# Performance work log

Measured on AMD Instinct MI355X. Metric: run time of the kernel, lower is better.

## Reference

```python
import jax, jax.numpy as jnp
import numpy as np

N_NODES = 50000
N_EDGES = 1600000
IN_CH = 128
HEADS = 4
OUT_PER_HEAD = 32  # out_channels // heads with concat=True
NEG_SLOPE = 0.2    # GATConv default leaky_relu slope
SOFTMAX_EPS = 1e-16  # PyG scatter-softmax denominator eps
LN_EPS = 1e-5


def setup_inputs() -> dict:
    key = jax.random.key(0)
    ks = jax.random.split(key, 8)
    x = jax.random.normal(ks[0], (N_NODES, IN_CH), dtype=jnp.float32)
    edge_index = jax.random.randint(ks[1], (2, N_EDGES), 0, N_NODES, dtype=jnp.int32)
    W = jax.random.normal(ks[2], (IN_CH, HEADS * OUT_PER_HEAD), dtype=jnp.float32) * (1.0 / np.sqrt(IN_CH))
    att_src = jax.random.normal(ks[3], (HEADS, OUT_PER_HEAD), dtype=jnp.float32) * 0.1
    att_dst = jax.random.normal(ks[4], (HEADS, OUT_PER_HEAD), dtype=jnp.float32) * 0.1
    bias = jnp.zeros((HEADS * OUT_PER_HEAD,), dtype=jnp.float32)
    gamma = jnp.ones((HEADS * OUT_PER_HEAD,), dtype=jnp.float32)
    beta = jnp.zeros((HEADS * OUT_PER_HEAD,), dtype=jnp.float32)
    return {"x": x, "edge_index": edge_index, "W": W, "att_src": att_src,
            "att_dst": att_dst, "bias": bias, "gamma": gamma, "beta": beta}


def reference(x, edge_index, W, att_src, att_dst, bias, gamma, beta):
    N = x.shape[0]
    H, C = att_src.shape
    # GATConv default add_self_loops=True
    loop = jnp.arange(N, dtype=edge_index.dtype)
    src = jnp.concatenate([edge_index[0], loop])  # message source j
    dst = jnp.concatenate([edge_index[1], loop])  # aggregation target i

    h = (x @ W).reshape(N, H, C)                      # [N,H,C]
    a_s = jnp.einsum('nhc,hc->nh', h, att_src)        # [N,H]
    a_d = jnp.einsum('nhc,hc->nh', h, att_dst)        # [N,H]

    logits = jax.nn.leaky_relu(a_s[src] + a_d[dst], NEG_SLOPE)  # [E,H]
    # segment softmax over edges grouped by destination node
    m = jax.ops.segment_max(logits, dst, num_segments=N)        # [N,H]
    m = jnp.where(jnp.isfinite(m), m, 0.0)
    e = jnp.exp(logits - m[dst])
    s = jax.ops.segment_sum(e, dst, num_segments=N)             # [N,H]
    alpha = e / (s[dst] + SOFTMAX_EPS)                          # [E,H]

    msg = h[src] * alpha[:, :, None]                            # [E,H,C]
    out = jax.ops.segment_sum(msg, dst, num_segments=N)         # [N,H,C]
    out = out.reshape(N, H * C) + bias

    mu = out.mean(axis=-1, keepdims=True)
    var = ((out - mu) ** 2).mean(axis=-1, keepdims=True)
    y = (out - mu) / jnp.sqrt(var + LN_EPS) * gamma + beta
    return jax.nn.elu(y)
```

## Files before the change

### kernel.cpp

```cpp
#include <hip/hip_runtime.h>
#include <hip/hip_bf16.h>

typedef __hip_bfloat16 bf16;
typedef unsigned int u32;
typedef unsigned short u16;

constexpr int N   = 50000;
constexpr int E   = 1600000;
constexpr int C   = 128;
constexpr int H   = 4;
constexpr int NB  = 782;
constexpr int CAP = 2560;
constexpr int CHUNK = 4096;
constexpr float NEG  = 0.2f;
constexpr float SEPS = 1e-16f;
constexpr float LEPS = 1e-5f;

__device__ __forceinline__ float lo16(u32 v) { return __uint_as_float(v << 16); }
__device__ __forceinline__ float hi16(u32 v) { return __uint_as_float(v & 0xFFFF0000u); }

__global__ __launch_bounds__(256) void k1_gemm(
    const float* __restrict__ x, const float* __restrict__ W,
    const float* __restrict__ att_s, const float* __restrict__ att_d,
    bf16* __restrict__ hb, float* __restrict__ as_, float* __restrict__ ad_)
{
    const int nb = blockIdx.x * 16;
    const int t  = threadIdx.x;
    __shared__ float sx[16 * 128];
    const float4* xg = (const float4*)(x + nb * 128);
    ((float4*)sx)[t]       = xg[t];
    ((float4*)sx)[t + 256] = xg[t + 256];
    __syncthreads();

    const int c = t & 127;
    const int g = t >> 7;
    const float* xb = sx + (g << 10);
    float acc[8] = {0.f, 0.f, 0.f, 0.f, 0.f, 0.f, 0.f, 0.f};

    for (int k = 0; k < 128; k += 4) {
        const float w0 = W[(k + 0) * 128 + c];
        const float w1 = W[(k + 1) * 128 + c];
        const float w2 = W[(k + 2) * 128 + c];
        const float w3 = W[(k + 3) * 128 + c];
#pragma unroll
        for (int j = 0; j < 8; ++j) {
            const float4 xv = *(const float4*)(xb + j * 128 + k);
            acc[j] = fmaf(xv.x, w0, fmaf(xv.y, w1, fmaf(xv.z, w2, fmaf(xv.w, w3, acc[j]))));
        }
    }

    const int lane = t & 63;
    const int head = c >> 5;
    const float asc = att_s[c], adc = att_d[c];
#pragma unroll
    for (int j = 0; j < 8; ++j) {
        const int node = nb + (g << 3) + j;
        hb[node * 128 + c] = __float2bfloat16(acc[j]);
        float vs = acc[j] * asc;
        float vd = acc[j] * adc;
#pragma unroll
        for (int off = 16; off; off >>= 1) {
            vs += __shfl_xor(vs, off, 64);
            vd += __shfl_xor(vd, off, 64);
        }
        if ((lane & 31) == 0) {
            as_[node * H + head] = vs;
            ad_[node * H + head] = vd;
        }
    }
}

__global__ __launch_bounds__(256) void kbin(
    const int* __restrict__ ei, u32* __restrict__ gcur, u32* __restrict__ pairs)
{
    __shared__ u32 lcnt[NB], lbase[NB], lfill[NB];
    const int t = threadIdx.x;
    const int base = blockIdx.x * CHUNK;
    const int nE = min(CHUNK, E - base);
    for (int i = t; i < NB; i += 256) lcnt[i] = 0;
    __syncthreads();
    for (int i = t; i < nE; i += 256)
        atomicAdd(&lcnt[((u32)ei[E + base + i]) >> 6], 1u);
    __syncthreads();
    for (int i = t; i < NB; i += 256) {
        u32 cb = lcnt[i];
        lbase[i] = cb ? atomicAdd(&gcur[i], cb) : 0u;
        lfill[i] = 0u;
    }
    __syncthreads();
    for (int i = t; i < nE; i += 256) {
        u32 src = (u32)ei[base + i];
        u32 dst = (u32)ei[E + base + i];
        u32 b = dst >> 6;
        u32 pos = atomicAdd(&lfill[b], 1u);
        pairs[(size_t)b * CAP + lbase[b] + pos] = src | ((dst & 63u) << 16);
    }
}

__global__ __launch_bounds__(64) void kscan(
    const u32* __restrict__ gcur, u32* __restrict__ bbase, int* __restrict__ row_ptr)
{
    const int t = threadIdx.x;
    u32 vals[13];
    u32 s = 0;
#pragma unroll
    for (int i = 0; i < 13; ++i) {
        int idx = t * 13 + i;
        u32 v = (idx < NB) ? gcur[idx] : 0u;
        vals[i] = s; s += v;
    }
    u32 incl = s;
#pragma unroll
    for (int off = 1; off < 64; off <<= 1) {
        u32 u = __shfl_up(incl, off, 64);
        if (t >= off) incl += u;
    }
    const u32 excl = incl - s;
#pragma unroll
    for (int i = 0; i < 13; ++i) {
        int idx = t * 13 + i;
        if (idx < NB) bbase[idx] = excl + vals[i];
    }
    if (t == 0) row_ptr[N] = E;
}

__global__ __launch_bounds__(256) void kfill2(
    const u32* __restrict__ pairs, const u32* __restrict__ gcur,
    const u32* __restrict__ bbase, int* __restrict__ row_ptr, u16* __restrict__ col)
{
    __shared__ int jcnt[64], joff[64], jcur[64];
    const int b = blockIdx.x, t = threadIdx.x;
    const int cntb = (int)gcur[b];
    const int base = (int)bbase[b];
    if (t < 64) jcnt[t] = 0;
    __syncthreads();
    const u32* pr = pairs + (size_t)b * CAP;
    for (int i = t; i < cntb; i += 256) atomicAdd(&jcnt[pr[i] >> 16], 1);
    __syncthreads();
    if (t < 64) {
        int v = jcnt[t], incl = v;
#pragma unroll
        for (int off = 1; off < 64; off <<= 1) {
            int u = __shfl_up(incl, off, 64);
            if (t >= off) incl += u;
        }
        joff[t] = incl - v;
        const int n = b * 64 + t;
        if (n < N) row_ptr[n] = base + joff[t];
        jcur[t] = 0;
    }
    __syncthreads();
    for (int i = t; i < cntb; i += 256) {
        const u32 p = pr[i];
        const int j = p >> 16;
        const int pos = atomicAdd(&jcur[j], 1);
        col[base + joff[j] + pos] = (u16)(p & 0xFFFFu);
    }
}

__global__ __launch_bounds__(256) void kd_agg_ln(
    const int* __restrict__ row_ptr, const u16* __restrict__ col,
    const u32* __restrict__ hb, const float* __restrict__ as_,
    const float* __restrict__ ad_,
    const float* __restrict__ bias, const float* __restrict__ gamma,
    const float* __restrict__ beta, float* __restrict__ out)
{
    int gid = blockIdx.x * blockDim.x + threadIdx.x;
    int n = gid >> 6;
    if (n >= N) return;
    const int lane = gid & 63;
    const int head = lane >> 4;

    const float adn = ad_[n * H + head];
    float l = as_[n * H + head] + adn;
    l = fmaxf(l, NEG * l);
    float w = __expf(l);
    float den = w;
    u32 hv = hb[n * 64 + lane];
    float num0 = w * lo16(hv);
    float num1 = w * hi16(hv);

    int k = row_ptr[n];
    const int end = row_ptr[n + 1];
    for (; k + 4 <= end; k += 4) {
        const int s0 = col[k], s1 = col[k + 1], s2 = col[k + 2], s3 = col[k + 3];
        float l0 = as_[s0 * H + head] + adn;
        float l1 = as_[s1 * H + head] + adn;
        float l2 = as_[s2 * H + head] + adn;
        float l3 = as_[s3 * H + head] + adn;
        const u32 v0 = hb[s0 * 64 + lane];
        const u32 v1 = hb[s1 * 64 + lane];
        const u32 v2 = hb[s2 * 64 + lane];
        const u32 v3 = hb[s3 * 64 + lane];
        l0 = fmaxf(l0, NEG * l0); l1 = fmaxf(l1, NEG * l1);
        l2 = fmaxf(l2, NEG * l2); l3 = fmaxf(l3, NEG * l3);
        const float w0 = __expf(l0), w1 = __expf(l1);
        const float w2 = __expf(l2), w3 = __expf(l3);
        den += (w0 + w1) + (w2 + w3);
        num0 = fmaf(w0, lo16(v0), num0); num1 = fmaf(w0, hi16(v0), num1);
        num0 = fmaf(w1, lo16(v1), num0); num1 = fmaf(w1, hi16(v1), num1);
        num0 = fmaf(w2, lo16(v2), num0); num1 = fmaf(w2, hi16(v2), num1);
        num0 = fmaf(w3, lo16(v3), num0); num1 = fmaf(w3, hi16(v3), num1);
    }
    for (; k < end; ++k) {
        const int s = col[k];
        float ls = as_[s * H + head] + adn;
        ls = fmaxf(ls, NEG * ls);
        const float ws = __expf(ls);
        const u32 vs = hb[s * 64 + lane];
        den += ws;
        num0 = fmaf(ws, lo16(vs), num0);
        num1 = fmaf(ws, hi16(vs), num1);
    }

    const int c0 = lane * 2;
    const float inv_den = 1.f / (den + SEPS);
    float v0 = num0 * inv_den + bias[c0];
    float v1 = num1 * inv_den + bias[c0 + 1];

    float sum = v0 + v1;
#pragma unroll
    for (int off = 32; off; off >>= 1) sum += __shfl_xor(sum, off, 64);
    const float mu = sum * (1.0f / C);
    const float d0 = v0 - mu, d1 = v1 - mu;
    float sq = d0 * d0 + d1 * d1;
#pragma unroll
    for (int off = 32; off; off >>= 1) sq += __shfl_xor(sq, off, 64);
    const float inv = rsqrtf(sq * (1.0f / C) + LEPS);
    float y0 = d0 * inv * gamma[c0]     + beta[c0];
    float y1 = d1 * inv * gamma[c0 + 1] + beta[c0 + 1];
    y0 = y0 > 0.f ? y0 : __expf(y0) - 1.f;
    y1 = y1 > 0.f ? y1 : __expf(y1) - 1.f;
    float2 o; o.x = y0; o.y = y1;
    *(float2*)(out + (size_t)n * C + c0) = o;
}

extern "C" void kernel_launch(void* const* d_in, const int* in_sizes, int n_in,
                              void* d_out, int out_size, void* d_ws, size_t ws_size,
                              hipStream_t stream)
{
    const float* x     = (const float*)d_in[0];
    const int*   ei    = (const int*)  d_in[1];
    const float* W     = (const float*)d_in[2];
    const float* att_s = (const float*)d_in[3];
    const float* att_d = (const float*)d_in[4];
    const float* bias  = (const float*)d_in[5];
    const float* gamma = (const float*)d_in[6];
    const float* beta  = (const float*)d_in[7];
    float* out = (float*)d_out;

    char* p = (char*)d_ws;
    bf16*  hb      = (bf16*)p;   p += (size_t)N * C * sizeof(bf16);
    float* as_     = (float*)p;  p += (size_t)N * H * sizeof(float);
    float* ad_     = (float*)p;  p += (size_t)N * H * sizeof(float);
    u32*   pairs   = (u32*)p;    p += (size_t)NB * CAP * sizeof(u32);
    u16*   col     = (u16*)p;    p += ((size_t)E * sizeof(u16) + 15) & ~(size_t)15;
    int*   row_ptr = (int*)p;    p += ((size_t)(N + 1) * sizeof(int) + 15) & ~(size_t)15;
    u32*   gcur    = (u32*)p;    p += (size_t)NB * sizeof(u32);
    u32*   bbase   = (u32*)p;

    hipMemsetAsync(gcur, 0, NB * sizeof(u32), stream);
    k1_gemm<<<N / 16, 256, 0, stream>>>(x, W, att_s, att_d, hb, as_, ad_);
    kbin<<<(E + CHUNK - 1) / CHUNK, 256, 0, stream>>>(ei, gcur, pairs);
    kscan<<<1, 64, 0, stream>>>(gcur, bbase, row_ptr);
    kfill2<<<NB, 256, 0, stream>>>(pairs, gcur, bbase, row_ptr, col);
    kd_agg_ln<<<(N * 64) / 256, 256, 0, stream>>>(
        row_ptr, col, (const u32*)hb, as_, ad_, bias, gamma, beta, out);
}
```

Baseline: 245.4 us.

## Precompute per-edge attention weights in CSR fill and fold scan into fill kernel

The CSR fill kernel now computes the leaky-relu/exp attention weight for all four heads of each edge and stores them as fp16 next to the column index, so the aggregation kernel only gathers a weight instead of recomputing it per lane. The separate scan kernel is removed; each fill block sums the preceding bucket counts itself. The binning kernel caches destinations in shared memory instead of reading them twice, and the aggregation loop is unrolled to 8 edges. This trades an extra E*8-byte write and read plus fp16 rounding of the weights for less exp work and fewer scattered as_ gathers in the hot kernel.

```diff
diff --git a/kernel.cpp b/kernel.cpp
--- a/kernel.cpp
+++ b/kernel.cpp
@@ -1,9 +1,11 @@
 #include <hip/hip_runtime.h>
 #include <hip/hip_bf16.h>
+#include <hip/hip_fp16.h>
 
 typedef __hip_bfloat16 bf16;
 typedef unsigned int u32;
 typedef unsigned short u16;
+typedef unsigned long long u64;
 
 constexpr int N   = 50000;
 constexpr int E   = 1600000;
@@ -74,13 +76,17 @@
     const int* __restrict__ ei, u32* __restrict__ gcur, u32* __restrict__ pairs)
 {
     __shared__ u32 lcnt[NB], lbase[NB], lfill[NB];
+    __shared__ u16 dstl[CHUNK];
     const int t = threadIdx.x;
     const int base = blockIdx.x * CHUNK;
     const int nE = min(CHUNK, E - base);
     for (int i = t; i < NB; i += 256) lcnt[i] = 0;
     __syncthreads();
-    for (int i = t; i < nE; i += 256)
-        atomicAdd(&lcnt[((u32)ei[E + base + i]) >> 6], 1u);
+    for (int i = t; i < nE; i += 256) {
+        u32 d = (u32)ei[E + base + i];
+        dstl[i] = (u16)d;
+        atomicAdd(&lcnt[d >> 6], 1u);
+    }
     __syncthreads();
     for (int i = t; i < NB; i += 256) {
         u32 cb = lcnt[i];
@@ -90,50 +96,39 @@
     __syncthreads();
     for (int i = t; i < nE; i += 256) {
         u32 src = (u32)ei[base + i];
-        u32 dst = (u32)ei[E + base + i];
+        u32 dst = (u32)dstl[i];
         u32 b = dst >> 6;
         u32 pos = atomicAdd(&lfill[b], 1u);
         pairs[(size_t)b * CAP + lbase[b] + pos] = src | ((dst & 63u) << 16);
     }
 }
 
-__global__ __launch_bounds__(64) void kscan(
-    const u32* __restrict__ gcur, u32* __restrict__ bbase, int* __restrict__ row_ptr)
-{
-    const int t = threadIdx.x;
-    u32 vals[13];
-    u32 s = 0;
-#pragma unroll
-    for (int i = 0; i < 13; ++i) {
-        int idx = t * 13 + i;
-        u32 v = (idx < NB) ? gcur[idx] : 0u;
-        vals[i] = s; s += v;
-    }
-    u32 incl = s;
-#pragma unroll
-    for (int off = 1; off < 64; off <<= 1) {
-        u32 u = __shfl_up(incl, off, 64);
-        if (t >= off) incl += u;
-    }
-    const u32 excl = incl - s;
-#pragma unroll
-    for (int i = 0; i < 13; ++i) {
-        int idx = t * 13 + i;
-        if (idx < NB) bbase[idx] = excl + vals[i];
-    }
-    if (t == 0) row_ptr[N] = E;
-}
-
 __global__ __launch_bounds__(256) void kfill2(
     const u32* __restrict__ pairs, const u32* __restrict__ gcur,
-    const u32* __restrict__ bbase, int* __restrict__ row_ptr, u16* __restrict__ col)
+    const float4* __restrict__ as4, const float4* __restrict__ ad4,
+    int* __restrict__ row_ptr, u16* __restrict__ col, __half* __restrict__ whf)
 {
     __shared__ int jcnt[64], joff[64], jcur[64];
+    __shared__ float4 adl[64];
+    __shared__ u32 ssum[4];
     const int b = blockIdx.x, t = threadIdx.x;
+    const int wave = t >> 6, lane = t & 63;
     const int cntb = (int)gcur[b];
-    const int base = (int)bbase[b];
-    if (t < 64) jcnt[t] = 0;
-    __syncthreads();
+
+    u32 part = 0;
+    for (int i = t; i < b; i += 256) part += gcur[i];
+#pragma unroll
+    for (int off = 32; off; off >>= 1) part += __shfl_xor(part, off, 64);
+    if (lane == 0) ssum[wave] = part;
+    if (t < 64) {
+        jcnt[t] = 0;
+        const int n = b * 64 + t;
+        adl[t] = (n < N) ? ad4[n] : make_float4(0.f, 0.f, 0.f, 0.f);
+    }
+    if (b == 0 && t == 255) row_ptr[N] = E;
+    __syncthreads();
+    const int base = (int)(ssum[0] + ssum[1] + ssum[2] + ssum[3]);
+
     const u32* pr = pairs + (size_t)b * CAP;
     for (int i = t; i < cntb; i += 256) atomicAdd(&jcnt[pr[i] >> 16], 1);
     __syncthreads();
@@ -153,15 +148,26 @@
     for (int i = t; i < cntb; i += 256) {
         const u32 p = pr[i];
         const int j = p >> 16;
+        const u32 s = p & 0xFFFFu;
         const int pos = atomicAdd(&jcur[j], 1);
-        col[base + joff[j] + pos] = (u16)(p & 0xFFFFu);
+        const int idx = base + joff[j] + pos;
+        col[idx] = (u16)s;
+        const float4 a = as4[s];
+        const float4 d = adl[j];
+        float l0 = a.x + d.x, l1 = a.y + d.y, l2 = a.z + d.z, l3 = a.w + d.w;
+        l0 = fmaxf(l0, NEG * l0); l1 = fmaxf(l1, NEG * l1);
+        l2 = fmaxf(l2, NEG * l2); l3 = fmaxf(l3, NEG * l3);
+        __half2 w01; w01.x = __float2half(__expf(l0)); w01.y = __float2half(__expf(l1));
+        __half2 w23; w23.x = __float2half(__expf(l2)); w23.y = __float2half(__expf(l3));
+        *(__half2*)(whf + (size_t)idx * 4)     = w01;
+        *(__half2*)(whf + (size_t)idx * 4 + 2) = w23;
     }
 }
 
 __global__ __launch_bounds__(256) void kd_agg_ln(
     const int* __restrict__ row_ptr, const u16* __restrict__ col,
-    const u32* __restrict__ hb, const float* __restrict__ as_,
-    const float* __restrict__ ad_,
+    const __half* __restrict__ whf, const u32* __restrict__ hb,
+    const float* __restrict__ as_, const float* __restrict__ ad_,
     const float* __restrict__ bias, const float* __restrict__ gamma,
     const float* __restrict__ beta, float* __restrict__ out)
 {
@@ -171,8 +177,7 @@
     const int lane = gid & 63;
     const int head = lane >> 4;
 
-    const float adn = ad_[n * H + head];
-    float l = as_[n * H + head] + adn;
+    float l = as_[n * H + head] + ad_[n * H + head];
     l = fmaxf(l, NEG * l);
     float w = __expf(l);
     float den = w;
@@ -182,31 +187,24 @@
 
     int k = row_ptr[n];
     const int end = row_ptr[n + 1];
-    for (; k + 4 <= end; k += 4) {
-        const int s0 = col[k], s1 = col[k + 1], s2 = col[k + 2], s3 = col[k + 3];
-        float l0 = as_[s0 * H + head] + adn;
-        float l1 = as_[s1 * H + head] + adn;
-        float l2 = as_[s2 * H + head] + adn;
-        float l3 = as_[s3 * H + head] + adn;
-        const u32 v0 = hb[s0 * 64 + lane];
-        const u32 v1 = hb[s1 * 64 + lane];
-        const u32 v2 = hb[s2 * 64 + lane];
-        const u32 v3 = hb[s3 * 64 + lane];
-        l0 = fmaxf(l0, NEG * l0); l1 = fmaxf(l1, NEG * l1);
-        l2 = fmaxf(l2, NEG * l2); l3 = fmaxf(l3, NEG * l3);
-        const float w0 = __expf(l0), w1 = __expf(l1);
-        const float w2 = __expf(l2), w3 = __expf(l3);
-        den += (w0 + w1) + (w2 + w3);
-        num0 = fmaf(w0, lo16(v0), num0); num1 = fmaf(w0, hi16(v0), num1);
-        num0 = fmaf(w1, lo16(v1), num0); num1 = fmaf(w1, hi16(v1), num1);
-        num0 = fmaf(w2, lo16(v2), num0); num1 = fmaf(w2, hi16(v2), num1);
-        num0 = fmaf(w3, lo16(v3), num0); num1 = fmaf(w3, hi16(v3), num1);
+    for (; k + 8 <= end; k += 8) {
+        int   s[8]; float ww[8]; u32 v[8];
+#pragma unroll
+        for (int i = 0; i < 8; ++i) s[i] = col[k + i];
+#pragma unroll
+        for (int i = 0; i < 8; ++i) ww[i] = __half2float(whf[(size_t)(k + i) * 4 + head]);
+#pragma unroll
+        for (int i = 0; i < 8; ++i) v[i] = hb[s[i] * 64 + lane];
+#pragma unroll
+        for (int i = 0; i < 8; ++i) {
+            den += ww[i];
+            num0 = fmaf(ww[i], lo16(v[i]), num0);
+            num1 = fmaf(ww[i], hi16(v[i]), num1);
+        }
     }
     for (; k < end; ++k) {
         const int s = col[k];
-        float ls = as_[s * H + head] + adn;
-        ls = fmaxf(ls, NEG * ls);
-        const float ws = __expf(ls);
+        const float ws = __half2float(whf[(size_t)k * 4 + head]);
         const u32 vs = hb[s * 64 + lane];
         den += ws;
         num0 = fmaf(ws, lo16(vs), num0);
@@ -250,20 +248,20 @@
     float* out = (float*)d_out;
 
     char* p = (char*)d_ws;
-    bf16*  hb      = (bf16*)p;   p += (size_t)N * C * sizeof(bf16);
-    float* as_     = (float*)p;  p += (size_t)N * H * sizeof(float);
-    float* ad_     = (float*)p;  p += (size_t)N * H * sizeof(float);
-    u32*   pairs   = (u32*)p;    p += (size_t)NB * CAP * sizeof(u32);
-    u16*   col     = (u16*)p;    p += ((size_t)E * sizeof(u16) + 15) & ~(size_t)15;
-    int*   row_ptr = (int*)p;    p += ((size_t)(N + 1) * sizeof(int) + 15) & ~(size_t)15;
-    u32*   gcur    = (u32*)p;    p += (size_t)NB * sizeof(u32);
-    u32*   bbase   = (u32*)p;
+    bf16*   hb      = (bf16*)p;   p += (size_t)N * C * sizeof(bf16);
+    float*  as_     = (float*)p;  p += (size_t)N * H * sizeof(float);
+    float*  ad_     = (float*)p;  p += (size_t)N * H * sizeof(float);
+    u32*    pairs   = (u32*)p;    p += (size_t)NB * CAP * sizeof(u32);
+    u16*    col     = (u16*)p;    p += ((size_t)E * sizeof(u16) + 15) & ~(size_t)15;
+    __half* whf     = (__half*)p; p += (size_t)E * 4 * sizeof(__half);
+    int*    row_ptr = (int*)p;    p += ((size_t)(N + 1) * sizeof(int) + 15) & ~(size_t)15;
+    u32*    gcur    = (u32*)p;
 
     hipMemsetAsync(gcur, 0, NB * sizeof(u32), stream);
     k1_gemm<<<N / 16, 256, 0, stream>>>(x, W, att_s, att_d, hb, as_, ad_);
     kbin<<<(E + CHUNK - 1) / CHUNK, 256, 0, stream>>>(ei, gcur, pairs);
-    kscan<<<1, 64, 0, stream>>>(gcur, bbase, row_ptr);
-    kfill2<<<NB, 256, 0, stream>>>(pairs, gcur, bbase, row_ptr, col);
+    kfill2<<<NB, 256, 0, stream>>>(pairs, gcur, (const float4*)as_,
+                                   (const float4*)ad_, row_ptr, col, whf);
     kd_agg_ln<<<(N * 64) / 256, 256, 0, stream>>>(
-        row_ptr, col, (const u32*)hb, as_, ad_, bias, gamma, beta, out);
-}
+        row_ptr, col, whf, (const u32*)hb, as_, ad_, bias, gamma, beta, out);
+}
```

Result: no change. 245.8 us (+0.2%).
